# Optimization experiments

Hardware: AMD Instinct MI355X
Metric: run time of the kernel (lower is better)

The kernel has to match this reference:

```python
import jax, jax.numpy as jnp
import numpy as np

NORM = 32768.0      # norm = 2**15 from init
SUBSTEPS = 8        # fixed Tsit5 substeps per saved group (replaces adaptive PID controller)

# Tsit5 (Tsitouras 2011) coefficients
A21 = 0.161
A31, A32 = -0.008480655492356989, 0.335480655492357
A41, A42, A43 = 2.8971530571054935, -6.359448489975075, 4.3622954328695815
A51, A52, A53, A54 = 5.325864828439257, -11.748883564062828, 7.4955393428898365, -0.09249506636175525
A61, A62, A63, A64, A65 = 5.86145544294642, -12.92096931784711, 8.159367898576159, -0.071584973281401, -0.028269050394068383
B1, B2, B3, B4, B5, B6 = 0.09646076681806523, 0.01, 0.4798896504144996, 1.379008574103742, -3.290069515436081, 2.324710524099774


def downsample_sum(x, n):
    # dLux downsample with mean=False: sum over n x n blocks
    H, W = x.shape
    return x.reshape(H // n, n, W // n, n).sum(axis=(1, 3))


def setup_inputs() -> dict:
    key = jax.random.key(0)
    illuminance = jax.random.uniform(key, (4096, 4096), dtype=jnp.float32) * 1000.0
    return {"illuminance": illuminance, "ngroups": 32}


def reference(illuminance, ngroups):
    # predict_ramp: normalize, initial downsample (oversample=1 -> factor 4)
    I = downsample_sum(illuminance / NORM, 4)  # [1024, 1024]

    def deriv(y):
        # ODEFunc.derivative: saturating detector ramp, autonomous in t
        return I * (1.0 - y)

    dt = 1.0 / (ngroups * SUBSTEPS)

    def tsit5_step(y, _):
        k1 = deriv(y)
        k2 = deriv(y + dt * (A21 * k1))
        k3 = deriv(y + dt * (A31 * k1 + A32 * k2))
        k4 = deriv(y + dt * (A41 * k1 + A42 * k2 + A43 * k3))
        k5 = deriv(y + dt * (A51 * k1 + A52 * k2 + A53 * k3 + A54 * k4))
        k6 = deriv(y + dt * (A61 * k1 + A62 * k2 + A63 * k3 + A64 * k4 + A65 * k5))
        y_new = y + dt * (B1 * k1 + B2 * k2 + B3 * k3 + B4 * k4 + B5 * k5 + B6 * k6)
        return y_new, None

    def group_step(y, _):
        y, _ = jax.lax.scan(tsit5_step, y, None, length=SUBSTEPS)
        return y, y  # save state at ts = (g+1)/ngroups

    y0 = jnp.zeros_like(I)
    _, ys = jax.lax.scan(group_step, y0, None, length=ngroups)  # [ngroups, 1024, 1024]

    # final_downsample is identity for oversample=1; undo normalization
    return NORM * ys
```

## Files before the change

kernel.cpp:

```cpp
#include <hip/hip_runtime.h>
#include <hip/hip_bf16.h>

#define A21 0.161f
#define A31 (-0.008480655492356989f)
#define A32 0.335480655492357f
#define A41 2.8971530571054935f
#define A42 (-6.359448489975075f)
#define A43 4.3622954328695815f
#define A51 5.325864828439257f
#define A52 (-11.748883564062828f)
#define A53 7.4955393428898365f
#define A54 (-0.09249506636175525f)
#define A61 5.86145544294642f
#define A62 (-12.92096931784711f)
#define A63 8.159367898576159f
#define A64 (-0.071584973281401f)
#define A65 (-0.028269050394068383f)
#define B1 0.09646076681806523f
#define B2 0.01f
#define B3 0.4798896504144996f
#define B4 1.379008574103742f
#define B5 (-3.290069515436081f)
#define B6 2.324710524099774f

#define NORM 32768.0f
#define SUBSTEPS 8
#define IN_DIM 4096
#define OUT_DIM 1024

__global__ __launch_bounds__(256) void ODERamp_kernel(
    const float* __restrict__ in,
    const int* __restrict__ ng_ptr,
    float* __restrict__ out)
{
    const int idx = blockIdx.x * blockDim.x + threadIdx.x;
    const int r = idx >> 10;
    const int c = idx & 1023;

    float s = 0.0f;
#pragma unroll
    for (int i = 0; i < 4; ++i) {
        const float4 v = *reinterpret_cast<const float4*>(
            in + (size_t)(4 * r + i) * IN_DIM + 4 * c);
        s += (v.x + v.y) + (v.z + v.w);
    }

    const int ngroups = *ng_ptr;
    const float I  = s * (1.0f / NORM);
    const float dt = 1.0f / (float)(ngroups * SUBSTEPS);
    const float z  = I * dt;

    const float q2 = 1.0f - A21 * z;
    const float q3 = 1.0f - z * (A31 + A32 * q2);
    const float q4 = 1.0f - z * (A41 + A42 * q2 + A43 * q3);
    const float q5 = 1.0f - z * (A51 + A52 * q2 + A53 * q3 + A54 * q4);
    const float q6 = 1.0f - z * (A61 + A62 * q2 + A63 * q3 + A64 * q4 + A65 * q5);
    const float R  = z * (B1 + B2 * q2 + B3 * q3 + B4 * q4 + B5 * q5 + B6 * q6);

    const float f  = 1.0f - R;
    const float f2 = f * f;
    const float f4 = f2 * f2;
    const float f8 = f4 * f4;

    float acc = 1.0f;
    for (int g = 0; g < ngroups; ++g) {
        acc *= f8;
        out[(size_t)g * (OUT_DIM * OUT_DIM) + idx] = NORM * (1.0f - acc);
    }
}

extern "C" void kernel_launch(void* const* d_in, const int* in_sizes, int n_in,
                              void* d_out, int out_size, void* d_ws, size_t ws_size,
                              hipStream_t stream) {
    const float* illum = (const float*)d_in[0];
    const int* ng = (const int*)d_in[1];
    float* out = (float*)d_out;

    const int n_pix = OUT_DIM * OUT_DIM;
    const int block = 256;
    const int grid = n_pix / block;

    ODERamp_kernel<<<grid, block, 0, stream>>>(illum, ng, out);
}
```

Before: 34.48 us.

## Split into downsample and vectorized expand kernels via workspace f8 field

Splits the single kernel into two. The first computes the per-pixel Tsit5 decay factor and writes it to a workspace buffer. The second reads four factors per thread and writes 16-byte vectorized stores for every group plane. This targets the write-dominated output with wider stores and fewer threads doing the store loop, at the cost of an extra launch and a 4 MB workspace round-trip.

```diff
diff --git a/kernel.cpp b/kernel.cpp
--- a/kernel.cpp
+++ b/kernel.cpp
@@ -28,10 +28,12 @@
 #define IN_DIM 4096
 #define OUT_DIM 1024
 
-__global__ __launch_bounds__(256) void ODERamp_kernel(
+typedef float f32x4 __attribute__((ext_vector_type(4)));
+
+__global__ __launch_bounds__(256) void ODERamp_downsample(
     const float* __restrict__ in,
     const int* __restrict__ ng_ptr,
-    float* __restrict__ out)
+    float* __restrict__ f8_field)
 {
     const int idx = blockIdx.x * blockDim.x + threadIdx.x;
     const int r = idx >> 10;
@@ -40,32 +42,50 @@
     float s = 0.0f;
 #pragma unroll
     for (int i = 0; i < 4; ++i) {
-        const float4 v = *reinterpret_cast<const float4*>(
+        const f32x4 v = *reinterpret_cast<const f32x4*>(
             in + (size_t)(4 * r + i) * IN_DIM + 4 * c);
         s += (v.x + v.y) + (v.z + v.w);
     }
 
     const int ngroups = *ng_ptr;
-    const float I  = s * (1.0f / NORM);
     const float dt = 1.0f / (float)(ngroups * SUBSTEPS);
-    const float z  = I * dt;
 
+    const float z  = s * (1.0f / NORM) * dt;
     const float q2 = 1.0f - A21 * z;
     const float q3 = 1.0f - z * (A31 + A32 * q2);
     const float q4 = 1.0f - z * (A41 + A42 * q2 + A43 * q3);
     const float q5 = 1.0f - z * (A51 + A52 * q2 + A53 * q3 + A54 * q4);
     const float q6 = 1.0f - z * (A61 + A62 * q2 + A63 * q3 + A64 * q4 + A65 * q5);
     const float R  = z * (B1 + B2 * q2 + B3 * q3 + B4 * q4 + B5 * q5 + B6 * q6);
-
     const float f  = 1.0f - R;
     const float f2 = f * f;
     const float f4 = f2 * f2;
-    const float f8 = f4 * f4;
+    f8_field[idx] = f4 * f4;
+}
 
-    float acc = 1.0f;
+__global__ __launch_bounds__(256) void ODERamp_expand(
+    const float* __restrict__ f8_field,
+    const int* __restrict__ ng_ptr,
+    float* __restrict__ out)
+{
+    const int t = blockIdx.x * blockDim.x + threadIdx.x;
+    const int p = t << 2;
+
+    const f32x4 f8 = *reinterpret_cast<const f32x4*>(f8_field + p);
+    const int ngroups = *ng_ptr;
+
+    float a0 = 1.0f, a1 = 1.0f, a2 = 1.0f, a3 = 1.0f;
+    f32x4* outp = reinterpret_cast<f32x4*>(out + p);
+    const size_t plane4 = (size_t)(OUT_DIM * OUT_DIM) / 4;
     for (int g = 0; g < ngroups; ++g) {
-        acc *= f8;
-        out[(size_t)g * (OUT_DIM * OUT_DIM) + idx] = NORM * (1.0f - acc);
+        a0 *= f8.x; a1 *= f8.y; a2 *= f8.z; a3 *= f8.w;
+        f32x4 o;
+        o.x = NORM - NORM * a0;
+        o.y = NORM - NORM * a1;
+        o.z = NORM - NORM * a2;
+        o.w = NORM - NORM * a3;
+        *outp = o;
+        outp += plane4;
     }
 }
 
@@ -75,10 +95,11 @@
     const float* illum = (const float*)d_in[0];
     const int* ng = (const int*)d_in[1];
     float* out = (float*)d_out;
+    float* f8_field = (float*)d_ws;
 
     const int n_pix = OUT_DIM * OUT_DIM;
     const int block = 256;
-    const int grid = n_pix / block;
 
-    ODERamp_kernel<<<grid, block, 0, stream>>>(illum, ng, out);
+    ODERamp_downsample<<<n_pix / block, block, 0, stream>>>(illum, ng, f8_field);
+    ODERamp_expand<<<(n_pix / 4) / block, block, 0, stream>>>(f8_field, ng, out);
 }
```

Measured after the change: 41.32 us. 19.8% more time.
